# Performance work log

Measured on AMD Instinct MI355X. Metric: run time of the kernel, lower is better.

The kernel has to match this reference:

```python
import jax, jax.numpy as jnp
import numpy as np

B, L, C, H = 4, 4096, 1024, 16
D = C // H  # head_dim = 64
EPS = 1e-6


def make_rope_tables(seq_len, head_dim, base=10000.0):
    inv_freq = 1.0 / (base ** (np.arange(0, head_dim, 2, dtype=np.float32) / head_dim))
    angles = np.arange(seq_len, dtype=np.float32)[:, None] * inv_freq[None, :]  # [L, D/2]
    angles = np.concatenate([angles, angles], axis=-1)  # [L, D]
    return jnp.asarray(np.cos(angles)), jnp.asarray(np.sin(angles))


def setup_inputs() -> dict:
    key = jax.random.key(0)
    ks = jax.random.split(key, 4)
    x = jax.random.normal(ks[0], (B, L, C), dtype=jnp.float32)
    W_qkv = jax.random.normal(ks[1], (3 * C, C), dtype=jnp.float32) * (C ** -0.5)
    q_scale = jnp.ones((D,), dtype=jnp.float32)
    k_scale = jnp.ones((D,), dtype=jnp.float32)
    W_proj = jax.random.normal(ks[2], (C, C), dtype=jnp.float32) * (C ** -0.5)
    b_proj = jnp.zeros((C,), dtype=jnp.float32)
    cos, sin = make_rope_tables(L, D)
    return {"x": x, "W_qkv": W_qkv, "q_scale": q_scale, "k_scale": k_scale,
            "W_proj": W_proj, "b_proj": b_proj, "cos": cos, "sin": sin}


def rms_norm(t, scale):
    # mean over last dim in fp32, like torch .mean(dtype=float32)
    ms = jnp.mean(jnp.square(t).astype(jnp.float32), axis=-1, keepdims=True)
    inv = jax.lax.rsqrt(ms + EPS).astype(t.dtype)
    return t * inv * scale.astype(t.dtype)


def rotate_half(t):
    t1, t2 = jnp.split(t, 2, axis=-1)
    return jnp.concatenate([-t2, t1], axis=-1)


def apply_rope(t, cos, sin):
    # t: [B, L, H, D]; cos/sin: [L, D]
    c = cos[None, :, None, :]
    s = sin[None, :, None, :]
    return t * c + rotate_half(t) * s


def reference(x, W_qkv, q_scale, k_scale, W_proj, b_proj, cos, sin):
    qkv = jnp.einsum('blc,ec->ble', x, W_qkv).reshape(B, L, 3, H, D)
    q, k, v = qkv[:, :, 0], qkv[:, :, 1], qkv[:, :, 2]  # [B, L, H, D]
    q = rms_norm(q, q_scale)
    k = rms_norm(k, k_scale)
    q = apply_rope(q, cos, sin)
    k = apply_rope(k, cos, sin)
    # scaled dot-product attention, non-causal
    scale = D ** -0.5
    scores = jnp.einsum('bqhd,bkhd->bhqk', q, k) * scale
    attn = jax.nn.softmax(scores, axis=-1)
    out = jnp.einsum('bhqk,bkhd->bqhd', attn, v).reshape(B, L, C)
    return out @ W_proj.T + b_proj
```

## Files before the change

kernel.cpp:

```cpp
#include <hip/hip_runtime.h>
#include <hip/hip_bf16.h>
#include <math.h>

#define B_ 4
#define L_ 4096
#define C_ 1024
#define H_ 16
#define D_ 64
#define C3_ 3072
#define EPS_ 1e-6f
#define QK_SCALE 0.18033688011112042f

typedef unsigned short u16;
typedef __attribute__((ext_vector_type(8))) short short8_t;
typedef __attribute__((ext_vector_type(4))) short short4_t;
typedef __attribute__((ext_vector_type(4))) float f32x4;

typedef const __attribute__((address_space(1))) void* gas_t;
typedef __attribute__((address_space(3))) void* las_t;

__device__ __forceinline__ void glds16(const void* g, void* l) {
  __builtin_amdgcn_global_load_lds((gas_t)g, (las_t)l, 16, 0, 0);
}

__device__ __forceinline__ u16 f2bf_u(float f) {
  __bf16 h = (__bf16)f;
  union { __bf16 b; u16 s; } u; u.b = h; return u.s;
}
__device__ __forceinline__ float bf2f_u(u16 s) {
  union { unsigned u; float f; } u2; u2.u = ((unsigned)s) << 16; return u2.f;
}

__global__ __launch_bounds__(256)
void split_kernel(const float* __restrict__ x, u16* __restrict__ hi,
                  u16* __restrict__ lo, int n4) {
  int i = blockIdx.x * 256 + threadIdx.x;
  const int stride = gridDim.x * 256;
  for (; i < n4; i += stride) {
    float4 v = ((const float4*)x)[i];
    short4_t h4, l4;
    h4[0] = f2bf_u(v.x); l4[0] = f2bf_u(v.x - bf2f_u(h4[0]));
    h4[1] = f2bf_u(v.y); l4[1] = f2bf_u(v.y - bf2f_u(h4[1]));
    h4[2] = f2bf_u(v.z); l4[2] = f2bf_u(v.z - bf2f_u(h4[2]));
    h4[3] = f2bf_u(v.w); l4[3] = f2bf_u(v.w - bf2f_u(h4[3]));
    ((short4_t*)hi)[i] = h4;
    ((short4_t*)lo)[i] = l4;
  }
}

template <int MODE>
__global__ __launch_bounds__(256)
void gemm_bx3_kernel(const u16* __restrict__ Ah, const u16* __restrict__ Al,
                     const u16* __restrict__ Bh, const u16* __restrict__ Bl,
                     const float* __restrict__ bias, float* __restrict__ Cf,
                     u16* __restrict__ outq, u16* __restrict__ outk,
                     u16* __restrict__ outv, int M, int N, int K) {
  __shared__ __align__(16) u16 S[4][128][32];

  const int tid = threadIdx.x;
  const int m0 = blockIdx.y * 128;
  const int n0 = blockIdx.x * 128;
  const int w = tid >> 6, lane = tid & 63;
  const int wr = w >> 1, wc = w & 1;
  const int l15 = lane & 15, lg = lane >> 4;

  f32x4 acc[4][4];
#pragma unroll
  for (int i = 0; i < 4; ++i)
#pragma unroll
    for (int j = 0; j < 4; ++j) acc[i][j] = (f32x4){0.f, 0.f, 0.f, 0.f};

  const int r0 = tid >> 2,         c0 = (tid & 3) * 8;
  const int r1 = (256 + tid) >> 2, c1 = (tid & 3) * 8;
  char* const Sb = (char*)&S[0][0][0];
  const int woff = w * 1024;

  for (int k0 = 0; k0 < K; k0 += 32) {
    __syncthreads();
    {
      const size_t a0 = (size_t)(m0 + r0) * K + k0 + c0;
      const size_t a1 = (size_t)(m0 + r1) * K + k0 + c1;
      const size_t b0 = (size_t)(n0 + r0) * K + k0 + c0;
      const size_t b1 = (size_t)(n0 + r1) * K + k0 + c1;
      glds16(Ah + a0, Sb + 0 * 8192 + 0 * 4096 + woff);
      glds16(Ah + a1, Sb + 0 * 8192 + 1 * 4096 + woff);
      glds16(Al + a0, Sb + 1 * 8192 + 0 * 4096 + woff);
      glds16(Al + a1, Sb + 1 * 8192 + 1 * 4096 + woff);
      glds16(Bh + b0, Sb + 2 * 8192 + 0 * 4096 + woff);
      glds16(Bh + b1, Sb + 2 * 8192 + 1 * 4096 + woff);
      glds16(Bl + b0, Sb + 3 * 8192 + 0 * 4096 + woff);
      glds16(Bl + b1, Sb + 3 * 8192 + 1 * 4096 + woff);
    }
    __syncthreads();

    short8_t af[2][4], bfr[2][4];
#pragma unroll
    for (int m = 0; m < 4; ++m) {
      const int row = wr * 64 + m * 16 + l15;
      af[0][m] = *(const short8_t*)(Sb + 0 * 8192 + row * 64 + lg * 16);
      af[1][m] = *(const short8_t*)(Sb + 1 * 8192 + row * 64 + lg * 16);
    }
#pragma unroll
    for (int n = 0; n < 4; ++n) {
      const int row = wc * 64 + n * 16 + l15;
      bfr[0][n] = *(const short8_t*)(Sb + 2 * 8192 + row * 64 + lg * 16);
      bfr[1][n] = *(const short8_t*)(Sb + 3 * 8192 + row * 64 + lg * 16);
    }
#pragma unroll
    for (int m = 0; m < 4; ++m)
#pragma unroll
      for (int n = 0; n < 4; ++n) {
        acc[m][n] = __builtin_amdgcn_mfma_f32_16x16x32_bf16(af[0][m], bfr[0][n], acc[m][n], 0, 0, 0);
        acc[m][n] = __builtin_amdgcn_mfma_f32_16x16x32_bf16(af[0][m], bfr[1][n], acc[m][n], 0, 0, 0);
        acc[m][n] = __builtin_amdgcn_mfma_f32_16x16x32_bf16(af[1][m], bfr[0][n], acc[m][n], 0, 0, 0);
      }
  }

  if constexpr (MODE == 0) {
    float bb[4];
#pragma unroll
    for (int n = 0; n < 4; ++n) bb[n] = bias ? bias[n0 + wc * 64 + n * 16 + l15] : 0.f;
#pragma unroll
    for (int m = 0; m < 4; ++m)
#pragma unroll
      for (int r = 0; r < 4; ++r) {
        const int row = m0 + wr * 64 + m * 16 + lg * 4 + r;
        float* orow = Cf + (size_t)row * N + n0 + wc * 64 + l15;
#pragma unroll
        for (int n = 0; n < 4; ++n) orow[n * 16] = acc[m][n][r] + bb[n];
      }
  } else {
    const int colbase = n0 + wc * 64;
    const int t = colbase >> 10;
    const int h = (colbase & 1023) >> 6;
    u16* const base = (t == 0) ? outq : (t == 1) ? outk : outv;
#pragma unroll
    for (int m = 0; m < 4; ++m)
#pragma unroll
      for (int r = 0; r < 4; ++r) {
        const int row = m0 + wr * 64 + m * 16 + lg * 4 + r;
        const int b = row >> 12, l = row & 4095;
        u16* dp = base + (((size_t)(b * H_ + h)) * L_ + l) * D_ + l15;
#pragma unroll
        for (int n = 0; n < 4; ++n) dp[n * 16] = f2bf_u(acc[m][n][r]);
      }
  }
}

__global__ __launch_bounds__(256)
void normrope2_kernel(u16* __restrict__ qb, u16* __restrict__ kb,
                      const float* __restrict__ q_scale,
                      const float* __restrict__ k_scale,
                      const float* __restrict__ cosT,
                      const float* __restrict__ sinT) {
  const int w = threadIdx.x >> 6, lane = threadIdx.x & 63;
  const int NR = B_ * H_ * L_;
  const int rid = blockIdx.x * 4 + w;
  const int isK = rid >= NR;
  const int r = rid - (isK ? NR : 0);
  const int l = r & (L_ - 1);

  u16* p = (isK ? kb : qb) + (size_t)r * D_ + lane;
  const float v = bf2f_u(*p);

  float ss = v * v;
#pragma unroll
  for (int off = 32; off; off >>= 1) ss += __shfl_xor(ss, off);
  const float inv = rsqrtf(ss * (1.0f / 64.0f) + EPS_);

  const float t = v * inv * (isK ? k_scale[lane] : q_scale[lane]);
  const float partner = __shfl_xor(t, 32);
  const float rot = (lane < 32) ? -partner : partner;
  float res = t * cosT[l * D_ + lane] + rot * sinT[l * D_ + lane];
  if (!isK) res *= QK_SCALE;
  *p = f2bf_u(res);
}

__global__ __launch_bounds__(256)
void vtrans_kernel(const u16* __restrict__ vb, u16* __restrict__ vt) {
  __shared__ __align__(16) u16 T[64][72];
  const int bh = blockIdx.y;
  const int l0 = blockIdx.x * 64;
  const int tid = threadIdx.x;
#pragma unroll
  for (int it = 0; it < 2; ++it) {
    const int idx = it * 256 + tid;
    const int l = idx >> 3, dc = idx & 7;
    short8_t v8 = *(const short8_t*)(vb + ((size_t)bh * L_ + l0 + l) * D_ + dc * 8);
#pragma unroll
    for (int j = 0; j < 8; ++j) T[dc * 8 + j][l] = (u16)v8[j];
  }
  __syncthreads();
#pragma unroll
  for (int it = 0; it < 2; ++it) {
    const int idx = it * 256 + tid;
    const int d = idx >> 3, q = idx & 7;
    short8_t o8 = *(const short8_t*)((const char*)&T[0][0] + d * 144 + q * 16);
    *(short8_t*)(vt + ((size_t)bh * D_ + d) * L_ + l0 + q * 8) = o8;
  }
}

__global__ __launch_bounds__(256)
void attn2_kernel(const u16* __restrict__ qb, const u16* __restrict__ kb,
                  const u16* __restrict__ vt, float* __restrict__ ctx) {
  __shared__ __align__(16) u16 Ks[64][64];
  __shared__ __align__(16) u16 Vs[64][64];
  __shared__ __align__(16) u16 Pt[4][16][88];

  const int bid0 = blockIdx.x;
  const int bid = (bid0 & 7) * 256 + (bid0 >> 3);
  const int qc = bid & 31;
  const int h  = (bid >> 5) & (H_ - 1);
  const int b  = bid >> 9;
  const int bh = b * H_ + h;

  const int tid = threadIdx.x;
  const int w = tid >> 6, lane = tid & 63;
  const int l15 = lane & 15, lg = lane >> 4;
  const int qrow0 = qc * 128 + w * 32;

  short8_t qf[2][2];
#pragma unroll
  for (int s = 0; s < 2; ++s)
#pragma unroll
    for (int kc = 0; kc < 2; ++kc)
      qf[s][kc] = *(const short8_t*)(qb + ((size_t)bh * L_ + qrow0 + s * 16 + l15) * D_ + kc * 32 + lg * 8);

  f32x4 O[2][4];
  float m_[2][4], l_[2][4];
#pragma unroll
  for (int s = 0; s < 2; ++s) {
#pragma unroll
    for (int nb = 0; nb < 4; ++nb) O[s][nb] = (f32x4){0.f, 0.f, 0.f, 0.f};
#pragma unroll
    for (int r = 0; r < 4; ++r) { m_[s][r] = -1e30f; l_[s][r] = 0.f; }
  }

  const u16* const kbase = kb + (size_t)bh * L_ * D_;
  const u16* const vbase = vt + (size_t)bh * D_ * L_;
  const int swoff = w * 1024;

  for (int k0 = 0; k0 < L_; k0 += 64) {
    __syncthreads();
#pragma unroll
    for (int it = 0; it < 2; ++it) {
      const int idx = it * 256 + tid;
      const int row = idx >> 3, ps = idx & 7;
      const int ls = ps ^ (row & 7);
      glds16(kbase + (size_t)(k0 + row) * D_ + ls * 8, (char*)&Ks[0][0] + it * 4096 + swoff);
      glds16(vbase + (size_t)row * L_ + k0 + ls * 8,   (char*)&Vs[0][0] + it * 4096 + swoff);
    }
    __syncthreads();

    short8_t pa[2][2];
#pragma unroll
    for (int s = 0; s < 2; ++s) {
      f32x4 a[4];
#pragma unroll
      for (int kb_ = 0; kb_ < 4; ++kb_) a[kb_] = (f32x4){0.f, 0.f, 0.f, 0.f};
#pragma unroll
      for (int kb_ = 0; kb_ < 4; ++kb_) {
        const int row = kb_ * 16 + l15;
        const short8_t kf0 = *(const short8_t*)((const char*)&Ks[0][0] + row * 128 + ((lg ^ (row & 7)) * 16));
        const short8_t kf1 = *(const short8_t*)((const char*)&Ks[0][0] + row * 128 + (((4 + lg) ^ (row & 7)) * 16));
        a[kb_] = __builtin_amdgcn_mfma_f32_16x16x32_bf16(qf[s][0], kf0, a[kb_], 0, 0, 0);
        a[kb_] = __builtin_amdgcn_mfma_f32_16x16x32_bf16(qf[s][1], kf1, a[kb_], 0, 0, 0);
      }
#pragma unroll
      for (int r = 0; r < 4; ++r) {
        float rm = fmaxf(fmaxf(a[0][r], a[1][r]), fmaxf(a[2][r], a[3][r]));
        rm = fmaxf(rm, __shfl_xor(rm, 1));
        rm = fmaxf(rm, __shfl_xor(rm, 2));
        rm = fmaxf(rm, __shfl_xor(rm, 4));
        rm = fmaxf(rm, __shfl_xor(rm, 8));
        const float mo = m_[s][r];
        const float mn = fmaxf(mo, rm);
        const float corr = exp2f(mo - mn);
        m_[s][r] = mn;
        float p0 = exp2f(a[0][r] - mn), p1 = exp2f(a[1][r] - mn);
        float p2 = exp2f(a[2][r] - mn), p3 = exp2f(a[3][r] - mn);
        float rs = (p0 + p1) + (p2 + p3);
        rs += __shfl_xor(rs, 1);
        rs += __shfl_xor(rs, 2);
        rs += __shfl_xor(rs, 4);
        rs += __shfl_xor(rs, 8);
        l_[s][r] = l_[s][r] * corr + rs;
#pragma unroll
        for (int nb = 0; nb < 4; ++nb) O[s][nb][r] *= corr;
        u16* prow = &Pt[w][lg * 4 + r][0];
        prow[l15]      = f2bf_u(p0);
        prow[16 + l15] = f2bf_u(p1);
        prow[32 + l15] = f2bf_u(p2);
        prow[48 + l15] = f2bf_u(p3);
      }
      pa[s][0] = *(const short8_t*)&Pt[w][l15][lg * 8];
      pa[s][1] = *(const short8_t*)&Pt[w][l15][32 + lg * 8];
    }

#pragma unroll
    for (int nb = 0; nb < 4; ++nb) {
      const int row = nb * 16 + l15;
#pragma unroll
      for (int kc = 0; kc < 2; ++kc) {
        const short8_t vf = *(const short8_t*)((const char*)&Vs[0][0] + row * 128 + (((kc * 4 + lg) ^ (row & 7)) * 16));
        O[0][nb] = __builtin_amdgcn_mfma_f32_16x16x32_bf16(pa[0][kc], vf, O[0][nb], 0, 0, 0);
        O[1][nb] = __builtin_amdgcn_mfma_f32_16x16x32_bf16(pa[1][kc], vf, O[1][nb], 0, 0, 0);
      }
    }
  }

#pragma unroll
  for (int s = 0; s < 2; ++s)
#pragma unroll
    for (int r = 0; r < 4; ++r) {
      const float inv = 1.0f / l_[s][r];
      float* cp = ctx + ((size_t)b * L_ + qrow0 + s * 16 + lg * 4 + r) * C_ + h * D_ + l15;
#pragma unroll
      for (int nb = 0; nb < 4; ++nb) cp[nb * 16] = O[s][nb][r] * inv;
    }
}

extern "C" void kernel_launch(void* const* d_in, const int* in_sizes, int n_in,
                              void* d_out, int out_size, void* d_ws, size_t ws_size,
                              hipStream_t stream) {
  const float* x       = (const float*)d_in[0];
  const float* W_qkv   = (const float*)d_in[1];
  const float* q_scale = (const float*)d_in[2];
  const float* k_scale = (const float*)d_in[3];
  const float* W_proj  = (const float*)d_in[4];
  const float* b_proj  = (const float*)d_in[5];
  const float* cosT    = (const float*)d_in[6];
  const float* sinT    = (const float*)d_in[7];
  float* out = (float*)d_out;

  const int M = B_ * L_;
  const size_t NBLH = (size_t)M * C_;

  u16* qb = (u16*)d_ws;
  u16* kb = qb + NBLH;
  u16* vb = kb + NBLH;
  u16* vt = vb + NBLH;
  float* ctx = (float*)((char*)d_ws + (size_t)128 * 1024 * 1024);
  u16* xh = (u16*)ctx;
  u16* xl = xh + NBLH;
  u16* wqh = (u16*)((char*)d_ws + (size_t)192 * 1024 * 1024);
  u16* wql = wqh + (size_t)C3_ * C_;
  u16* wph = wql + (size_t)C3_ * C_;
  u16* wpl = wph + (size_t)C_ * C_;
  u16* ch = qb;
  u16* cl = kb;

  split_kernel<<<2048, 256, 0, stream>>>(x, xh, xl, (int)(NBLH / 4));
  split_kernel<<<512, 256, 0, stream>>>(W_qkv, wqh, wql, C3_ * C_ / 4);
  split_kernel<<<512, 256, 0, stream>>>(W_proj, wph, wpl, C_ * C_ / 4);
  {
    dim3 grid(C3_ / 128, M / 128);
    gemm_bx3_kernel<1><<<grid, 256, 0, stream>>>(xh, xl, wqh, wql, nullptr,
                                                 nullptr, qb, kb, vb, M, C3_, C_);
  }
  normrope2_kernel<<<2 * B_ * H_ * L_ / 4, 256, 0, stream>>>(qb, kb, q_scale, k_scale, cosT, sinT);
  {
    dim3 grid(L_ / 64, B_ * H_);
    vtrans_kernel<<<grid, 256, 0, stream>>>(vb, vt);
  }
  attn2_kernel<<<B_ * H_ * (L_ / 128), 256, 0, stream>>>(qb, kb, vt, ctx);
  split_kernel<<<2048, 256, 0, stream>>>(ctx, ch, cl, (int)(NBLH / 4));
  {
    dim3 grid(C_ / 128, M / 128);
    gemm_bx3_kernel<0><<<grid, 256, 0, stream>>>(ch, cl, wph, wpl, b_proj, out,
                                                 nullptr, nullptr, nullptr, M, C_, C_);
  }
}
```

Measured before the change: 1.563 ms.

## Rework attention with 128-key tiles, transposed S, lazy rescale, fused bf16 split output

The attention kernel now processes 128 keys per iteration and computes S transposed (K as the A operand), so the row max and sum need only two cross-lane shuffles instead of four. It adds a lazy rescale: the running max and the O accumulators are updated only when some new max exceeds the stored one by more than 8 in log2 space. The context output is written directly as bf16 hi/lo pairs, which removes the fp32 ctx buffer and the separate split kernel. This costs more registers and LDS, and the lazy-rescale threshold allows larger unnormalised exponentials.

Result: faster. 1.300 ms (-16.8%).

```diff
diff --git a/kernel.cpp b/kernel.cpp
--- a/kernel.cpp
+++ b/kernel.cpp
@@ -201,11 +201,12 @@
 }
 
 __global__ __launch_bounds__(256)
-void attn2_kernel(const u16* __restrict__ qb, const u16* __restrict__ kb,
-                  const u16* __restrict__ vt, float* __restrict__ ctx) {
-  __shared__ __align__(16) u16 Ks[64][64];
-  __shared__ __align__(16) u16 Vs[64][64];
-  __shared__ __align__(16) u16 Pt[4][16][88];
+void attn3_kernel(const u16* __restrict__ qb, const u16* __restrict__ kb,
+                  const u16* __restrict__ vt, u16* __restrict__ ch,
+                  u16* __restrict__ cl) {
+  __shared__ __align__(16) u16 Ks[128][64];
+  __shared__ __align__(16) u16 Vs[64][128];
+  __shared__ __align__(16) u16 Pt[4][16][136];
 
   const int bid0 = blockIdx.x;
   const int bid = (bid0 & 7) * 256 + (bid0 >> 3);
@@ -227,97 +228,125 @@
       qf[s][kc] = *(const short8_t*)(qb + ((size_t)bh * L_ + qrow0 + s * 16 + l15) * D_ + kc * 32 + lg * 8);
 
   f32x4 O[2][4];
-  float m_[2][4], l_[2][4];
-#pragma unroll
-  for (int s = 0; s < 2; ++s) {
+#pragma unroll
+  for (int s = 0; s < 2; ++s)
 #pragma unroll
     for (int nb = 0; nb < 4; ++nb) O[s][nb] = (f32x4){0.f, 0.f, 0.f, 0.f};
-#pragma unroll
-    for (int r = 0; r < 4; ++r) { m_[s][r] = -1e30f; l_[s][r] = 0.f; }
-  }
+  float m0s = -1e30f, m1s = -1e30f;
+  float ll0 = 0.f, ll1 = 0.f;
 
   const u16* const kbase = kb + (size_t)bh * L_ * D_;
   const u16* const vbase = vt + (size_t)bh * D_ * L_;
-  const int swoff = w * 1024;
-
-  for (int k0 = 0; k0 < L_; k0 += 64) {
+
+  for (int k0 = 0; k0 < L_; k0 += 128) {
     __syncthreads();
 #pragma unroll
-    for (int it = 0; it < 2; ++it) {
+    for (int it = 0; it < 4; ++it) {
       const int idx = it * 256 + tid;
-      const int row = idx >> 3, ps = idx & 7;
-      const int ls = ps ^ (row & 7);
-      glds16(kbase + (size_t)(k0 + row) * D_ + ls * 8, (char*)&Ks[0][0] + it * 4096 + swoff);
-      glds16(vbase + (size_t)row * L_ + k0 + ls * 8,   (char*)&Vs[0][0] + it * 4096 + swoff);
+      const int rK = idx >> 3, pK = idx & 7;
+      glds16(kbase + (size_t)(k0 + rK) * D_ + ((pK ^ (rK & 7)) * 8),
+             (char*)&Ks[0][0] + it * 4096 + w * 1024);
+      const int rV = idx >> 4, pV = idx & 15;
+      glds16(vbase + (size_t)rV * L_ + k0 + ((pV ^ (rV & 7)) * 8),
+             (char*)&Vs[0][0] + it * 4096 + w * 1024);
     }
     __syncthreads();
 
-    short8_t pa[2][2];
-#pragma unroll
-    for (int s = 0; s < 2; ++s) {
-      f32x4 a[4];
-#pragma unroll
-      for (int kb_ = 0; kb_ < 4; ++kb_) a[kb_] = (f32x4){0.f, 0.f, 0.f, 0.f};
-#pragma unroll
-      for (int kb_ = 0; kb_ < 4; ++kb_) {
-        const int row = kb_ * 16 + l15;
-        const short8_t kf0 = *(const short8_t*)((const char*)&Ks[0][0] + row * 128 + ((lg ^ (row & 7)) * 16));
-        const short8_t kf1 = *(const short8_t*)((const char*)&Ks[0][0] + row * 128 + (((4 + lg) ^ (row & 7)) * 16));
-        a[kb_] = __builtin_amdgcn_mfma_f32_16x16x32_bf16(qf[s][0], kf0, a[kb_], 0, 0, 0);
-        a[kb_] = __builtin_amdgcn_mfma_f32_16x16x32_bf16(qf[s][1], kf1, a[kb_], 0, 0, 0);
-      }
-#pragma unroll
-      for (int r = 0; r < 4; ++r) {
-        float rm = fmaxf(fmaxf(a[0][r], a[1][r]), fmaxf(a[2][r], a[3][r]));
-        rm = fmaxf(rm, __shfl_xor(rm, 1));
-        rm = fmaxf(rm, __shfl_xor(rm, 2));
-        rm = fmaxf(rm, __shfl_xor(rm, 4));
-        rm = fmaxf(rm, __shfl_xor(rm, 8));
-        const float mo = m_[s][r];
-        const float mn = fmaxf(mo, rm);
-        const float corr = exp2f(mo - mn);
-        m_[s][r] = mn;
-        float p0 = exp2f(a[0][r] - mn), p1 = exp2f(a[1][r] - mn);
-        float p2 = exp2f(a[2][r] - mn), p3 = exp2f(a[3][r] - mn);
-        float rs = (p0 + p1) + (p2 + p3);
-        rs += __shfl_xor(rs, 1);
-        rs += __shfl_xor(rs, 2);
-        rs += __shfl_xor(rs, 4);
-        rs += __shfl_xor(rs, 8);
-        l_[s][r] = l_[s][r] * corr + rs;
-#pragma unroll
-        for (int nb = 0; nb < 4; ++nb) O[s][nb][r] *= corr;
-        u16* prow = &Pt[w][lg * 4 + r][0];
-        prow[l15]      = f2bf_u(p0);
-        prow[16 + l15] = f2bf_u(p1);
-        prow[32 + l15] = f2bf_u(p2);
-        prow[48 + l15] = f2bf_u(p3);
-      }
-      pa[s][0] = *(const short8_t*)&Pt[w][l15][lg * 8];
-      pa[s][1] = *(const short8_t*)&Pt[w][l15][32 + lg * 8];
-    }
+    f32x4 a0[8], a1[8];
+#pragma unroll
+    for (int kb_ = 0; kb_ < 8; ++kb_) {
+      a0[kb_] = (f32x4){0.f, 0.f, 0.f, 0.f};
+      a1[kb_] = (f32x4){0.f, 0.f, 0.f, 0.f};
+    }
+#pragma unroll
+    for (int kb_ = 0; kb_ < 8; ++kb_) {
+      const int row = kb_ * 16 + l15;
+      const short8_t kf0 = *(const short8_t*)((const char*)&Ks[0][0] + row * 128 + ((lg ^ (row & 7)) * 16));
+      const short8_t kf1 = *(const short8_t*)((const char*)&Ks[0][0] + row * 128 + (((4 + lg) ^ (row & 7)) * 16));
+      a0[kb_] = __builtin_amdgcn_mfma_f32_16x16x32_bf16(kf0, qf[0][0], a0[kb_], 0, 0, 0);
+      a0[kb_] = __builtin_amdgcn_mfma_f32_16x16x32_bf16(kf1, qf[0][1], a0[kb_], 0, 0, 0);
+      a1[kb_] = __builtin_amdgcn_mfma_f32_16x16x32_bf16(kf0, qf[1][0], a1[kb_], 0, 0, 0);
+      a1[kb_] = __builtin_amdgcn_mfma_f32_16x16x32_bf16(kf1, qf[1][1], a1[kb_], 0, 0, 0);
+    }
+
+    short8_t pa0[4], pa1[4];
+
+#define STRIP(A, MS, LLS, OS, PA)                                              \
+    {                                                                          \
+      f32x4 mx = A[0];                                                         \
+      _Pragma("unroll")                                                        \
+      for (int kb_ = 1; kb_ < 8; ++kb_) {                                      \
+        _Pragma("unroll")                                                      \
+        for (int r = 0; r < 4; ++r) mx[r] = fmaxf(mx[r], A[kb_][r]);           \
+      }                                                                        \
+      float rm = fmaxf(fmaxf(mx[0], mx[1]), fmaxf(mx[2], mx[3]));              \
+      rm = fmaxf(rm, __shfl_xor(rm, 16));                                      \
+      rm = fmaxf(rm, __shfl_xor(rm, 32));                                      \
+      if (__any(rm > MS + 8.0f)) {                                             \
+        const float mn = fmaxf(MS, rm);                                        \
+        const float corr = exp2f(MS - mn);                                     \
+        MS = mn;                                                               \
+        LLS *= corr;                                                           \
+        _Pragma("unroll")                                                      \
+        for (int r = 0; r < 4; ++r) {                                          \
+          const float cr = __shfl(corr, 4 * lg + r);                           \
+          _Pragma("unroll")                                                    \
+          for (int nb = 0; nb < 4; ++nb) OS[nb][r] *= cr;                      \
+        }                                                                      \
+      }                                                                        \
+      _Pragma("unroll")                                                        \
+      for (int kb_ = 0; kb_ < 8; ++kb_) {                                      \
+        const float p0 = exp2f(A[kb_][0] - MS);                                \
+        const float p1 = exp2f(A[kb_][1] - MS);                                \
+        const float p2 = exp2f(A[kb_][2] - MS);                                \
+        const float p3 = exp2f(A[kb_][3] - MS);                                \
+        LLS += (p0 + p1) + (p2 + p3);                                          \
+        short4_t pw;                                                           \
+        pw[0] = (short)f2bf_u(p0); pw[1] = (short)f2bf_u(p1);                  \
+        pw[2] = (short)f2bf_u(p2); pw[3] = (short)f2bf_u(p3);                  \
+        *(short4_t*)&Pt[w][l15][16 * kb_ + 4 * lg] = pw;                       \
+      }                                                                        \
+      _Pragma("unroll")                                                        \
+      for (int kc = 0; kc < 4; ++kc)                                           \
+        PA[kc] = *(const short8_t*)&Pt[w][l15][kc * 32 + lg * 8];              \
+    }
+
+    STRIP(a0, m0s, ll0, O[0], pa0)
+    STRIP(a1, m1s, ll1, O[1], pa1)
+#undef STRIP
 
 #pragma unroll
     for (int nb = 0; nb < 4; ++nb) {
       const int row = nb * 16 + l15;
 #pragma unroll
-      for (int kc = 0; kc < 2; ++kc) {
-        const short8_t vf = *(const short8_t*)((const char*)&Vs[0][0] + row * 128 + (((kc * 4 + lg) ^ (row & 7)) * 16));
-        O[0][nb] = __builtin_amdgcn_mfma_f32_16x16x32_bf16(pa[0][kc], vf, O[0][nb], 0, 0, 0);
-        O[1][nb] = __builtin_amdgcn_mfma_f32_16x16x32_bf16(pa[1][kc], vf, O[1][nb], 0, 0, 0);
+      for (int kc = 0; kc < 4; ++kc) {
+        const short8_t vf = *(const short8_t*)((const char*)&Vs[0][0] + row * 256 + (((kc * 4 + lg) ^ (row & 7)) * 16));
+        O[0][nb] = __builtin_amdgcn_mfma_f32_16x16x32_bf16(pa0[kc], vf, O[0][nb], 0, 0, 0);
+        O[1][nb] = __builtin_amdgcn_mfma_f32_16x16x32_bf16(pa1[kc], vf, O[1][nb], 0, 0, 0);
       }
     }
   }
 
 #pragma unroll
-  for (int s = 0; s < 2; ++s)
+  for (int s = 0; s < 2; ++s) {
+    float t = s ? ll1 : ll0;
+    t += __shfl_xor(t, 16);
+    t += __shfl_xor(t, 32);
+    const float inv = 1.0f / t;
 #pragma unroll
     for (int r = 0; r < 4; ++r) {
-      const float inv = 1.0f / l_[s][r];
-      float* cp = ctx + ((size_t)b * L_ + qrow0 + s * 16 + lg * 4 + r) * C_ + h * D_ + l15;
-#pragma unroll
-      for (int nb = 0; nb < 4; ++nb) cp[nb * 16] = O[s][nb][r] * inv;
-    }
+      const float invr = __shfl(inv, 4 * lg + r);
+      const int row = qrow0 + s * 16 + lg * 4 + r;
+      const size_t base = ((size_t)b * L_ + row) * C_ + h * D_ + l15;
+#pragma unroll
+      for (int nb = 0; nb < 4; ++nb) {
+        const float v = O[s][nb][r] * invr;
+        const u16 hv = f2bf_u(v);
+        ch[base + nb * 16] = hv;
+        cl[base + nb * 16] = f2bf_u(v - bf2f_u(hv));
+      }
+    }
+  }
 }
 
 extern "C" void kernel_launch(void* const* d_in, const int* in_sizes, int n_in,
@@ -340,15 +369,14 @@
   u16* kb = qb + NBLH;
   u16* vb = kb + NBLH;
   u16* vt = vb + NBLH;
-  float* ctx = (float*)((char*)d_ws + (size_t)128 * 1024 * 1024);
-  u16* xh = (u16*)ctx;
+  u16* xh = (u16*)((char*)d_ws + (size_t)128 * 1024 * 1024);
   u16* xl = xh + NBLH;
   u16* wqh = (u16*)((char*)d_ws + (size_t)192 * 1024 * 1024);
   u16* wql = wqh + (size_t)C3_ * C_;
   u16* wph = wql + (size_t)C3_ * C_;
   u16* wpl = wph + (size_t)C_ * C_;
-  u16* ch = qb;
-  u16* cl = kb;
+  u16* ch = xh;
+  u16* cl = xl;
 
   split_kernel<<<2048, 256, 0, stream>>>(x, xh, xl, (int)(NBLH / 4));
   split_kernel<<<512, 256, 0, stream>>>(W_qkv, wqh, wql, C3_ * C_ / 4);
@@ -363,8 +391,7 @@
     dim3 grid(L_ / 64, B_ * H_);
     vtrans_kernel<<<grid, 256, 0, stream>>>(vb, vt);
   }
-  attn2_kernel<<<B_ * H_ * (L_ / 128), 256, 0, stream>>>(qb, kb, vt, ctx);
-  split_kernel<<<2048, 256, 0, stream>>>(ctx, ch, cl, (int)(NBLH / 4));
+  attn3_kernel<<<B_ * H_ * (L_ / 128), 256, 0, stream>>>(qb, kb, vt, ch, cl);
   {
     dim3 grid(C_ / 128, M / 128);
     gemm_bx3_kernel<0><<<grid, 256, 0, stream>>>(ch, cl, wph, wpl, b_proj, out,
```
